# Optimization experiments

Hardware: AMD Instinct MI355X
Metric: run time of the kernel (lower is better)

Reference implementation:

```python
import jax, jax.numpy as jnp
import numpy as np

WS = 7           # window size
NH = 12          # num heads
EPS_ADA = 1e-6   # AdaLayerNorm eps
EPS_LN = 1e-5    # torch nn.LayerNorm default eps


def _rel_pos_index(ws):
    coords = np.stack(np.meshgrid(np.arange(ws), np.arange(ws), indexing='ij'))  # (2,ws,ws)
    flat = coords.reshape(2, -1)                      # (2, N)
    rel = flat[:, :, None] - flat[:, None, :]         # (2, N, N)
    rel = rel.transpose(1, 2, 0).astype(np.int64)     # (N, N, 2)
    rel[:, :, 0] += ws - 1
    rel[:, :, 1] += ws - 1
    rel[:, :, 0] *= 2 * ws - 1
    return jnp.asarray(rel.sum(-1))                   # (N, N) in [0, (2ws-1)^2)

REL_IDX = _rel_pos_index(WS)


def setup_inputs() -> dict:
    key = jax.random.key(0)
    ks = jax.random.split(key, 8)
    B, H, W, C, COND = 32, 56, 56, 384, 128
    L = H * W
    s = 0.02
    return {
        'x_tok': jax.random.normal(ks[0], (B, L, C), jnp.float32),
        'z_tok': jax.random.normal(ks[1], (B, L, C), jnp.float32),
        'cond': jax.random.normal(ks[2], (B, COND), jnp.float32),
        'gamma_x': jnp.ones((C,), jnp.float32),
        'beta_x': jnp.zeros((C,), jnp.float32),
        'mod_w': jax.random.normal(ks[3], (COND, 2 * C), jnp.float32) * s,
        'mod_b': jnp.zeros((2 * C,), jnp.float32),
        'gamma_z': jnp.ones((C,), jnp.float32),
        'beta_z': jnp.zeros((C,), jnp.float32),
        'rel_bias_table': jax.random.normal(ks[4], ((2 * WS - 1) ** 2, NH), jnp.float32) * s,
        'q_w': jax.random.normal(ks[5], (C, C), jnp.float32) * s,
        'q_b': jnp.zeros((C,), jnp.float32),
        'kv_w': jax.random.normal(ks[6], (C, 2 * C), jnp.float32) * s,
        'kv_b': jnp.zeros((2 * C,), jnp.float32),
        'proj_w': jax.random.normal(ks[7], (C, C), jnp.float32) * s,
        'proj_b': jnp.zeros((C,), jnp.float32),
        'H': H,
        'W': W,
    }


def reference(x_tok, z_tok, cond, gamma_x, beta_x, mod_w, mod_b,
              gamma_z, beta_z, rel_bias_table, q_w, q_b, kv_w, kv_b,
              proj_w, proj_b, H, W):
    B, L, C = x_tok.shape
    hd = C // NH
    N = WS * WS

    # AdaLayerNorm-Zero on x
    mu = x_tok.mean(-1, keepdims=True)
    var = ((x_tok - mu) ** 2).mean(-1, keepdims=True)
    x_hat = (x_tok - mu) * jax.lax.rsqrt(var + EPS_ADA)
    mod = (cond @ mod_w + mod_b).reshape(B, 2, C)
    d_gamma, d_beta = mod[:, 0], mod[:, 1]
    x = (gamma_x * (1.0 + d_gamma))[:, None, :] * x_hat + (beta_x + d_beta)[:, None, :]

    # LayerNorm on z
    mz = z_tok.mean(-1, keepdims=True)
    vz = ((z_tok - mz) ** 2).mean(-1, keepdims=True)
    z = (z_tok - mz) * jax.lax.rsqrt(vz + EPS_LN) * gamma_z + beta_z

    # window partition: (B,H,W,C) -> (B*nW, N, C)
    def part(t):
        t = t.reshape(B, H // WS, WS, W // WS, WS, C)
        return t.transpose(0, 1, 3, 2, 4, 5).reshape(-1, N, C)

    x_win = part(x.reshape(B, H, W, C))
    z_win = part(z.reshape(B, H, W, C))

    # cross window attention
    q = (x_win @ q_w + q_b).reshape(-1, N, NH, hd).transpose(0, 2, 1, 3)  # (Bw,H,N,d)
    kv = (z_win @ kv_w + kv_b).reshape(-1, N, 2, NH, hd)
    k = kv[:, :, 0].transpose(0, 2, 1, 3)
    v = kv[:, :, 1].transpose(0, 2, 1, 3)
    scale = hd ** -0.5
    attn = jnp.einsum('bhnd,bhmd->bhnm', q * scale, k)                    # (Bw,H,N,N)
    bias = rel_bias_table[REL_IDX.reshape(-1)].reshape(N, N, NH).transpose(2, 0, 1)
    attn = jax.nn.softmax(attn + bias[None], axis=-1)
    out = jnp.einsum('bhnm,bhmd->bhnd', attn, v).transpose(0, 2, 1, 3).reshape(-1, N, C)
    out = out @ proj_w + proj_b

    # window reverse: (B*nW, N, C) -> (B, L, C)
    fused = out.reshape(B, H // WS, W // WS, WS, WS, C)
    fused = fused.transpose(0, 1, 3, 2, 4, 5).reshape(B, L, C)

    return x_tok + fused
```

## Files before the change

### kernel.cpp

```cpp
#include <hip/hip_runtime.h>
#include <hip/hip_bf16.h>

typedef float f32x4 __attribute__((ext_vector_type(4)));
typedef short short8 __attribute__((ext_vector_type(8)));
typedef __hip_bfloat16 bf16;

constexpr int CDIM  = 384;
constexpr int LTOK  = 3136;
constexpr int NWIN  = 2048;
constexpr int MROWS = 100352;
constexpr int MPAD  = MROWS + 64;

__device__ __forceinline__ void gload_lds16(const void* g, void* l) {
  __builtin_amdgcn_global_load_lds(
      (const __attribute__((address_space(1))) void*)g,
      (__attribute__((address_space(3))) void*)l, 16, 0, 0);
}

__device__ __forceinline__ void row_to_bl(int r, int& b, int& l) {
  int w = r / 49, n = r % 49;
  b = w >> 6;
  int wrem = w & 63;
  int wy = wrem >> 3, wx = wrem & 7;
  int ny = n / 7, nx = n % 7;
  l = (wy * 7 + ny) * 56 + wx * 7 + nx;
}


__global__ __launch_bounds__(256) void mod_kernel(
    const float* __restrict__ cond, const float* __restrict__ mw,
    const float* __restrict__ mb, float* __restrict__ mod) {
  int idx = blockIdx.x * 256 + threadIdx.x;
  int b = idx / 768, j = idx % 768;
  float s = mb[j];
  const float* cr = cond + b * 128;
  #pragma unroll 4
  for (int k = 0; k < 128; k++) s += cr[k] * mw[(size_t)k * 768 + j];
  mod[idx] = s;
}

__global__ __launch_bounds__(256) void prep_wt(
    const float* __restrict__ qw, const float* __restrict__ kvw,
    const float* __restrict__ pw,
    bf16* __restrict__ wtq, bf16* __restrict__ wtkv, bf16* __restrict__ wtp) {
  int idx = blockIdx.x * 256 + threadIdx.x;
  const float* src; bf16* dst; int i, Wn;
  if (idx < 147456)      { i = idx;          src = qw;  dst = wtq;  Wn = 384; }
  else if (idx < 442368) { i = idx - 147456; src = kvw; dst = wtkv; Wn = 768; }
  else                   { i = idx - 442368; src = pw;  dst = wtp;  Wn = 384; }
  int j = i & 7, n = (i >> 3) & 63, g = (i >> 9) & 3;
  int kt = (i >> 11) % 12, chunk = i / 24576;
  int k = kt * 32 + g * 8 + j, ng = chunk * 64 + n;
  dst[i] = __float2bfloat16(src[(size_t)k * Wn + ng]);
}

__global__ __launch_bounds__(256) void bias_kernel(
    const float* __restrict__ tab, float* __restrict__ bT) {
  int idx = blockIdx.x * 256 + threadIdx.x;
  int h = idx >> 12, rem = idx & 4095, m = rem >> 6, c = rem & 63;
  float v;
  if (c >= 49)      v = -1e30f;
  else if (m >= 49) v = 0.f;
  else {
    int yq = m / 7, xq = m % 7, yk = c / 7, xk = c % 7;
    v = tab[((yq - yk + 6) * 13 + (xq - xk + 6)) * 12 + h];
  }
  bT[idx] = v;
}


struct alignas(8) B4 { bf16 h[4]; };

__global__ __launch_bounds__(256) void ln_kernel(
    const float* __restrict__ src, const float* __restrict__ gamma,
    const float* __restrict__ beta, const float* __restrict__ mod,
    float eps, bf16* __restrict__ dst) {
  int wid = threadIdx.x >> 6, lane = threadIdx.x & 63;
  int r = blockIdx.x * 4 + wid;
  int bb, ll; row_to_bl(r, bb, ll);
  const f32x4* x4 = (const f32x4*)(src + ((size_t)bb * LTOK + ll) * 384);
  f32x4 a = x4[lane];
  f32x4 b = {0.f, 0.f, 0.f, 0.f};
  if (lane < 32) b = x4[64 + lane];
  float s  = a[0] + a[1] + a[2] + a[3] + b[0] + b[1] + b[2] + b[3];
  float s2 = a[0]*a[0] + a[1]*a[1] + a[2]*a[2] + a[3]*a[3]
           + b[0]*b[0] + b[1]*b[1] + b[2]*b[2] + b[3]*b[3];
  #pragma unroll
  for (int d = 1; d < 64; d <<= 1) { s += __shfl_xor(s, d); s2 += __shfl_xor(s2, d); }
  float mu = s * (1.f / 384.f);
  float var = s2 * (1.f / 384.f) - mu * mu;
  float rstd = rsqrtf(var + eps);
  bf16* o = dst + (size_t)r * 384;
  const f32x4* g4 = (const f32x4*)gamma;
  const f32x4* be4 = (const f32x4*)beta;
  if (mod != nullptr) {
    const f32x4* mg4 = (const f32x4*)(mod + bb * 768);
    const f32x4* mb4 = (const f32x4*)(mod + bb * 768 + 384);
    {
      f32x4 gg = g4[lane], bb2 = be4[lane], mg = mg4[lane], mb = mb4[lane];
      B4 p;
      #pragma unroll
      for (int i = 0; i < 4; i++)
        p.h[i] = __float2bfloat16((gg[i] * (1.f + mg[i])) * ((a[i] - mu) * rstd) + bb2[i] + mb[i]);
      *((B4*)o + lane) = p;
    }
    if (lane < 32) {
      f32x4 gg = g4[64 + lane], bb2 = be4[64 + lane], mg = mg4[64 + lane], mb = mb4[64 + lane];
      B4 p;
      #pragma unroll
      for (int i = 0; i < 4; i++)
        p.h[i] = __float2bfloat16((gg[i] * (1.f + mg[i])) * ((b[i] - mu) * rstd) + bb2[i] + mb[i]);
      *((B4*)o + 64 + lane) = p;
    }
  } else {
    {
      f32x4 gg = g4[lane], bb2 = be4[lane];
      B4 p;
      #pragma unroll
      for (int i = 0; i < 4; i++)
        p.h[i] = __float2bfloat16((a[i] - mu) * rstd * gg[i] + bb2[i]);
      *((B4*)o + lane) = p;
    }
    if (lane < 32) {
      f32x4 gg = g4[64 + lane], bb2 = be4[64 + lane];
      B4 p;
      #pragma unroll
      for (int i = 0; i < 4; i++)
        p.h[i] = __float2bfloat16((b[i] - mu) * rstd * gg[i] + bb2[i]);
      *((B4*)o + 64 + lane) = p;
    }
  }
}


template<int MODE>
__global__ __launch_bounds__(256, 3) void gemm2(
    const bf16* __restrict__ A, const bf16* __restrict__ WTt,
    const float* __restrict__ bias, void* __restrict__ outp,
    const float* __restrict__ resid, float scale, int N) {
  __shared__ __align__(16) char Bs[49152];
  const int t = threadIdx.x;
  const int wid = t >> 6, lane = t & 63;
  const int r16 = lane & 15, g = lane >> 4;
  const int wr0 = blockIdx.x * 128 + wid * 32;

  short8 aF[2][12];
  #pragma unroll
  for (int m = 0; m < 2; m++)
    #pragma unroll
    for (int kt = 0; kt < 12; kt++)
      aF[m][kt] = *(const short8*)(A + (size_t)(wr0 + m * 16 + r16) * 384 + kt * 32 + g * 8);

  const int NCH = N >> 6;
  auto stage = [&](int c) {
    const char* srcp = (const char*)WTt + (size_t)c * 49152;
    #pragma unroll
    for (int i = 0; i < 12; i++)
      gload_lds16(srcp + (i * 256 + t) * 16, Bs + (i * 256 + t) * 16);
  };
  stage(0);

  for (int c = 0; c < NCH; c++) {
    __syncthreads();
    f32x4 acc[2][4] = {};
    #pragma unroll
    for (int kt = 0; kt < 12; kt++) {
      #pragma unroll
      for (int ni = 0; ni < 4; ni++) {
        short8 bF = *(const short8*)(Bs + kt * 4096 + g * 1024 + (ni * 16 + r16) * 16);
        acc[0][ni] = __builtin_amdgcn_mfma_f32_16x16x32_bf16(aF[0][kt], bF, acc[0][ni], 0, 0, 0);
        acc[1][ni] = __builtin_amdgcn_mfma_f32_16x16x32_bf16(aF[1][kt], bF, acc[1][ni], 0, 0, 0);
      }
    }
    __syncthreads();
    if (c + 1 < NCH) stage(c + 1);

    if (MODE == 0) {
      bf16* O = (bf16*)outp;
      #pragma unroll
      for (int ni = 0; ni < 4; ni++) {
        int col = c * 64 + ni * 16 + r16;
        float bc = bias[col];
        #pragma unroll
        for (int m = 0; m < 2; m++) {
          int row0 = wr0 + m * 16 + g * 4;
          #pragma unroll
          for (int rr = 0; rr < 4; rr++)
            O[(size_t)(row0 + rr) * N + col] = __float2bfloat16((acc[m][ni][rr] + bc) * scale);
        }
      }
    } else {
      float* O = (float*)outp;
      #pragma unroll
      for (int m = 0; m < 2; m++) {
        #pragma unroll
        for (int rr = 0; rr < 4; rr++) {
          int row = wr0 + m * 16 + g * 4 + rr;
          int bb, ll; row_to_bl(row, bb, ll);
          size_t base = ((size_t)bb * LTOK + ll) * 384;
          #pragma unroll
          for (int ni = 0; ni < 4; ni++) {
            int col = c * 64 + ni * 16 + r16;
            O[base + col] = resid[base + col] + acc[m][ni][rr] + bias[col];
          }
        }
      }
    }
  }
}


__global__ __launch_bounds__(64) void attn_kernel(
    const bf16* __restrict__ q, const bf16* __restrict__ kv,
    const float* __restrict__ biasT, bf16* __restrict__ o) {
  __shared__ __align__(16) bf16 vt[32][72];
  __shared__ __align__(16) bf16 P[64][72];
  const int h = blockIdx.x, w = blockIdx.y;
  const int lane = threadIdx.x;
  const int r16 = lane & 15, g = lane >> 4;
  const size_t qbase = (size_t)w * 49 * 384 + h * 32;
  const size_t kvbase = (size_t)w * 49 * 768 + h * 32;

  for (int e = lane; e < 32 * 72; e += 64) ((bf16*)vt)[e] = __float2bfloat16(0.f);
  for (int e = lane; e < 49 * 32; e += 64) {
    int c = e >> 5, d = e & 31;
    vt[d][c] = kv[kvbase + (size_t)c * 768 + 384 + d];
  }

  short8 aq[4], bk[4];
  #pragma unroll
  for (int mi = 0; mi < 4; mi++)
    aq[mi] = *(const short8*)(q + qbase + (size_t)(mi * 16 + r16) * 384 + g * 8);
  #pragma unroll
  for (int ni = 0; ni < 4; ni++)
    bk[ni] = *(const short8*)(kv + kvbase + (size_t)(ni * 16 + r16) * 768 + g * 8);

  f32x4 zero = {0.f, 0.f, 0.f, 0.f};
  f32x4 S[4][4];
  #pragma unroll
  for (int mi = 0; mi < 4; mi++)
    #pragma unroll
    for (int ni = 0; ni < 4; ni++)
      S[mi][ni] = __builtin_amdgcn_mfma_f32_16x16x32_bf16(aq[mi], bk[ni], zero, 0, 0, 0);

  const float* bt = biasT + h * 4096;
  #pragma unroll
  for (int mi = 0; mi < 4; mi++) {
    #pragma unroll
    for (int r = 0; r < 4; r++) {
      int rowm = mi * 16 + g * 4 + r;
      float sv[4];
      #pragma unroll
      for (int ni = 0; ni < 4; ni++)
        sv[ni] = S[mi][ni][r] + bt[rowm * 64 + ni * 16 + r16];
      float mx = fmaxf(fmaxf(sv[0], sv[1]), fmaxf(sv[2], sv[3]));
      #pragma unroll
      for (int d = 1; d < 16; d <<= 1) mx = fmaxf(mx, __shfl_xor(mx, d));
      float sum = 0.f;
      #pragma unroll
      for (int ni = 0; ni < 4; ni++) { sv[ni] = __expf(sv[ni] - mx); sum += sv[ni]; }
      #pragma unroll
      for (int d = 1; d < 16; d <<= 1) sum += __shfl_xor(sum, d);
      float inv = __fdividef(1.f, sum);
      #pragma unroll
      for (int ni = 0; ni < 4; ni++)
        P[rowm][ni * 16 + r16] = __float2bfloat16(sv[ni] * inv);
    }
  }
  __syncthreads();

  f32x4 acc[4][2] = {};
  #pragma unroll
  for (int c0 = 0; c0 < 2; c0++) {
    short8 ap[4], bv[2];
    #pragma unroll
    for (int mi = 0; mi < 4; mi++)
      ap[mi] = *(const short8*)((const char*)&P[0][0] + (mi * 16 + r16) * 144 + c0 * 64 + g * 16);
    #pragma unroll
    for (int di = 0; di < 2; di++)
      bv[di] = *(const short8*)((const char*)&vt[0][0] + (di * 16 + r16) * 144 + c0 * 64 + g * 16);
    #pragma unroll
    for (int mi = 0; mi < 4; mi++)
      #pragma unroll
      for (int di = 0; di < 2; di++)
        acc[mi][di] = __builtin_amdgcn_mfma_f32_16x16x32_bf16(ap[mi], bv[di], acc[mi][di], 0, 0, 0);
  }

  #pragma unroll
  for (int mi = 0; mi < 4; mi++) {
    #pragma unroll
    for (int r = 0; r < 4; r++) {
      int m = mi * 16 + g * 4 + r;
      if (m < 49) {
        #pragma unroll
        for (int di = 0; di < 2; di++)
          o[(size_t)(w * 49 + m) * 384 + h * 32 + di * 16 + r16] =
              __float2bfloat16(acc[mi][di][r]);
      }
    }
  }
}


extern "C" void kernel_launch(void* const* d_in, const int* in_sizes, int n_in,
                              void* d_out, int out_size, void* d_ws, size_t ws_size,
                              hipStream_t stream) {
  (void)in_sizes; (void)n_in; (void)out_size; (void)ws_size;
  const float* x_tok   = (const float*)d_in[0];
  const float* z_tok   = (const float*)d_in[1];
  const float* cond    = (const float*)d_in[2];
  const float* gamma_x = (const float*)d_in[3];
  const float* beta_x  = (const float*)d_in[4];
  const float* mod_w   = (const float*)d_in[5];
  const float* mod_b   = (const float*)d_in[6];
  const float* gamma_z = (const float*)d_in[7];
  const float* beta_z  = (const float*)d_in[8];
  const float* rel_tab = (const float*)d_in[9];
  const float* q_w     = (const float*)d_in[10];
  const float* q_b     = (const float*)d_in[11];
  const float* kv_w    = (const float*)d_in[12];
  const float* kv_b    = (const float*)d_in[13];
  const float* proj_w  = (const float*)d_in[14];
  const float* proj_b  = (const float*)d_in[15];

  char* ws = (char*)d_ws;
  float* modbuf = (float*)(ws + 0);
  bf16*  wtq    = (bf16*)(ws + 98304);
  bf16*  wtkv   = (bf16*)(ws + 98304 + 294912);
  bf16*  wtp    = (bf16*)(ws + 98304 + 294912 + 589824);
  float* biasT  = (float*)(ws + 98304 + 294912 + 589824 + 294912);
  char*  R1     = ws + 1474560;
  char*  R2     = R1 + (size_t)MPAD * 384 * 2;
  char*  R3     = R2 + (size_t)MPAD * 384 * 2;

  hipMemsetAsync(R2 + (size_t)MROWS * 384 * 2, 0, 64 * 384 * 2, stream);
  hipMemsetAsync(R3 + (size_t)MROWS * 768 * 2, 0, 64 * 768 * 2, stream);

  mod_kernel <<<96,   256, 0, stream>>>(cond, mod_w, mod_b, modbuf);
  prep_wt    <<<2304, 256, 0, stream>>>(q_w, kv_w, proj_w, wtq, wtkv, wtp);
  bias_kernel<<<192,  256, 0, stream>>>(rel_tab, biasT);

  ln_kernel<<<25088, 256, 0, stream>>>(x_tok, gamma_x, beta_x, modbuf, 1e-6f, (bf16*)R1);
  gemm2<0><<<784, 256, 0, stream>>>(
      (const bf16*)R1, wtq, q_b, R2, nullptr, 0.17677669529663687f, 384);
  ln_kernel<<<25088, 256, 0, stream>>>(z_tok, gamma_z, beta_z, nullptr, 1e-5f, (bf16*)R1);
  gemm2<0><<<784, 256, 0, stream>>>(
      (const bf16*)R1, wtkv, kv_b, R3, nullptr, 1.0f, 768);
  attn_kernel<<<dim3(12, NWIN), 64, 0, stream>>>(
      (const bf16*)R2, (const bf16*)R3, biasT, (bf16*)R1);
  gemm2<1><<<784, 256, 0, stream>>>(
      (const bf16*)R1, wtp, proj_b, d_out, x_tok, 1.0f, 384);
}
```

Baseline: 656.0 us.

## Double-buffer weight chunks in GEMM with 32-column tiles and LDS bias

The GEMM kernel now streams 32-column weight chunks into two alternating LDS buffers, prefetching the next chunk before computing the current one. Manual vmcnt waits and raw barriers replace the syncthreads pair, so the weight loads can overlap the MFMA work and the epilogue stores. The bias is also cached in LDS, and the weight-prep layout is changed to match the new chunking. The cost is more loop iterations with fewer MFMAs each, and vmcnt counts that must exactly match the number of outstanding epilogue stores.

```diff
diff --git a/kernel.cpp b/kernel.cpp
--- a/kernel.cpp
+++ b/kernel.cpp
@@ -48,10 +48,11 @@
   if (idx < 147456)      { i = idx;          src = qw;  dst = wtq;  Wn = 384; }
   else if (idx < 442368) { i = idx - 147456; src = kvw; dst = wtkv; Wn = 768; }
   else                   { i = idx - 442368; src = pw;  dst = wtp;  Wn = 384; }
-  int j = i & 7, n = (i >> 3) & 63, g = (i >> 9) & 3;
-  int kt = (i >> 11) % 12, chunk = i / 24576;
-  int k = kt * 32 + g * 8 + j, ng = chunk * 64 + n;
-  dst[i] = __float2bfloat16(src[(size_t)k * Wn + ng]);
+  int chunk = i / 12288, rem = i % 12288;
+  int kt = rem >> 10, rem2 = rem & 1023;
+  int ni = (rem2 >> 9) & 1, g = (rem2 >> 7) & 3, r16 = (rem2 >> 3) & 15, j = rem2 & 7;
+  int k = kt * 32 + g * 8 + j, n = chunk * 32 + ni * 16 + r16;
+  dst[i] = __float2bfloat16(src[(size_t)k * Wn + n]);
 }
 
 __global__ __launch_bounds__(256) void bias_kernel(
@@ -134,11 +135,12 @@
 
 
 template<int MODE>
-__global__ __launch_bounds__(256, 3) void gemm2(
+__global__ __launch_bounds__(256, 3) void gemm3(
     const bf16* __restrict__ A, const bf16* __restrict__ WTt,
     const float* __restrict__ bias, void* __restrict__ outp,
     const float* __restrict__ resid, float scale, int N) {
-  __shared__ __align__(16) char Bs[49152];
+  __shared__ __align__(16) char Bs[2][24576];
+  __shared__ float biasS[768];
   const int t = threadIdx.x;
   const int wid = t >> 6, lane = t & 63;
   const int r16 = lane & 15, g = lane >> 4;
@@ -151,36 +153,54 @@
     for (int kt = 0; kt < 12; kt++)
       aF[m][kt] = *(const short8*)(A + (size_t)(wr0 + m * 16 + r16) * 384 + kt * 32 + g * 8);
 
-  const int NCH = N >> 6;
-  auto stage = [&](int c) {
-    const char* srcp = (const char*)WTt + (size_t)c * 49152;
-    #pragma unroll
-    for (int i = 0; i < 12; i++)
-      gload_lds16(srcp + (i * 256 + t) * 16, Bs + (i * 256 + t) * 16);
+  #pragma unroll
+  for (int i = 0; i < 3; i++) {
+    int idx = i * 256 + t;
+    if (idx < N) biasS[idx] = bias[idx];
+  }
+
+  const int NCH = N >> 5;
+  auto stage = [&](int c, int pb) {
+    const char* srcp = (const char*)WTt + (size_t)c * 24576;
+    #pragma unroll
+    for (int i = 0; i < 6; i++)
+      gload_lds16(srcp + i * 4096 + t * 16, Bs[pb] + i * 4096 + t * 16);
   };
-  stage(0);
-
-  for (int c = 0; c < NCH; c++) {
-    __syncthreads();
-    f32x4 acc[2][4] = {};
+  stage(0, 0);
+  __syncthreads();
+
+  constexpr int EPI = (MODE == 0) ? 16 : 32;
+
+  for (int c = 0; c < NCH; ++c) {
+    if (c + 1 < NCH) {
+      stage(c + 1, (c + 1) & 1);
+      asm volatile("s_waitcnt vmcnt(%0)" :: "i"(EPI + 6) : "memory");
+    } else {
+      asm volatile("s_waitcnt vmcnt(%0)" :: "i"(EPI) : "memory");
+    }
+    __builtin_amdgcn_s_barrier();
+    __builtin_amdgcn_sched_barrier(0);
+
+    const char* bufp = Bs[c & 1];
+    f32x4 acc[2][2] = {};
     #pragma unroll
     for (int kt = 0; kt < 12; kt++) {
-      #pragma unroll
-      for (int ni = 0; ni < 4; ni++) {
-        short8 bF = *(const short8*)(Bs + kt * 4096 + g * 1024 + (ni * 16 + r16) * 16);
-        acc[0][ni] = __builtin_amdgcn_mfma_f32_16x16x32_bf16(aF[0][kt], bF, acc[0][ni], 0, 0, 0);
-        acc[1][ni] = __builtin_amdgcn_mfma_f32_16x16x32_bf16(aF[1][kt], bF, acc[1][ni], 0, 0, 0);
-      }
-    }
-    __syncthreads();
-    if (c + 1 < NCH) stage(c + 1);
+      short8 b0 = *(const short8*)(bufp + kt * 2048 + g * 256 + r16 * 16);
+      short8 b1 = *(const short8*)(bufp + kt * 2048 + 1024 + g * 256 + r16 * 16);
+      acc[0][0] = __builtin_amdgcn_mfma_f32_16x16x32_bf16(aF[0][kt], b0, acc[0][0], 0, 0, 0);
+      acc[1][0] = __builtin_amdgcn_mfma_f32_16x16x32_bf16(aF[1][kt], b0, acc[1][0], 0, 0, 0);
+      acc[0][1] = __builtin_amdgcn_mfma_f32_16x16x32_bf16(aF[0][kt], b1, acc[0][1], 0, 0, 0);
+      acc[1][1] = __builtin_amdgcn_mfma_f32_16x16x32_bf16(aF[1][kt], b1, acc[1][1], 0, 0, 0);
+    }
+    __builtin_amdgcn_sched_barrier(0);
+    __builtin_amdgcn_s_barrier();
 
     if (MODE == 0) {
       bf16* O = (bf16*)outp;
       #pragma unroll
-      for (int ni = 0; ni < 4; ni++) {
-        int col = c * 64 + ni * 16 + r16;
-        float bc = bias[col];
+      for (int ni = 0; ni < 2; ni++) {
+        int col = c * 32 + ni * 16 + r16;
+        float bc = biasS[col];
         #pragma unroll
         for (int m = 0; m < 2; m++) {
           int row0 = wr0 + m * 16 + g * 4;
@@ -199,9 +219,9 @@
           int bb, ll; row_to_bl(row, bb, ll);
           size_t base = ((size_t)bb * LTOK + ll) * 384;
           #pragma unroll
-          for (int ni = 0; ni < 4; ni++) {
-            int col = c * 64 + ni * 16 + r16;
-            O[base + col] = resid[base + col] + acc[m][ni][rr] + bias[col];
+          for (int ni = 0; ni < 2; ni++) {
+            int col = c * 32 + ni * 16 + r16;
+            O[base + col] = resid[base + col] + acc[m][ni][rr] + biasS[col];
           }
         }
       }
@@ -341,13 +361,13 @@
   bias_kernel<<<192,  256, 0, stream>>>(rel_tab, biasT);
 
   ln_kernel<<<25088, 256, 0, stream>>>(x_tok, gamma_x, beta_x, modbuf, 1e-6f, (bf16*)R1);
-  gemm2<0><<<784, 256, 0, stream>>>(
+  gemm3<0><<<784, 256, 0, stream>>>(
       (const bf16*)R1, wtq, q_b, R2, nullptr, 0.17677669529663687f, 384);
   ln_kernel<<<25088, 256, 0, stream>>>(z_tok, gamma_z, beta_z, nullptr, 1e-5f, (bf16*)R1);
-  gemm2<0><<<784, 256, 0, stream>>>(
+  gemm3<0><<<784, 256, 0, stream>>>(
       (const bf16*)R1, wtkv, kv_b, R3, nullptr, 1.0f, 768);
   attn_kernel<<<dim3(12, NWIN), 64, 0, stream>>>(
       (const bf16*)R2, (const bf16*)R3, biasT, (bf16*)R1);
-  gemm2<1><<<784, 256, 0, stream>>>(
+  gemm3<1><<<784, 256, 0, stream>>>(
       (const bf16*)R1, wtp, proj_b, d_out, x_tok, 1.0f, 384);
 }
```

Measured after the change: 614.4 us. 1.07x faster.

## Make GEMM blocks weight-stationary and merge prep and layernorm launches

Applied to the files above, without the earlier changes.

The GEMM is restructured so each block loads one 64-column weight slice into LDS once. It then loops persistently over 64-row panels of A, reading A fragments from global memory each iteration, instead of holding 128 rows of A in registers and streaming every weight chunk through LDS with barriers. The three prep kernels are merged into one launch, and the two layernorms into one launch writing separate buffers, which cuts launch count and lets the x and z normalizations run concurrently. The trade-off is that A is re-read from global memory once per column slice (6 or 12 times) instead of once, relying on L2 to absorb it, while occupancy rises to 4 blocks per CU.

```diff
diff --git a/kernel.cpp b/kernel.cpp
--- a/kernel.cpp
+++ b/kernel.cpp
@@ -10,6 +10,7 @@
 constexpr int NWIN  = 2048;
 constexpr int MROWS = 100352;
 constexpr int MPAD  = MROWS + 64;
+constexpr int NP64  = 1568;
 
 __device__ __forceinline__ void gload_lds16(const void* g, void* l) {
   __builtin_amdgcn_global_load_lds(
@@ -27,56 +28,67 @@
 }
 
 
-__global__ __launch_bounds__(256) void mod_kernel(
+__global__ __launch_bounds__(256) void prep_all(
     const float* __restrict__ cond, const float* __restrict__ mw,
-    const float* __restrict__ mb, float* __restrict__ mod) {
-  int idx = blockIdx.x * 256 + threadIdx.x;
-  int b = idx / 768, j = idx % 768;
-  float s = mb[j];
-  const float* cr = cond + b * 128;
-  #pragma unroll 4
-  for (int k = 0; k < 128; k++) s += cr[k] * mw[(size_t)k * 768 + j];
-  mod[idx] = s;
-}
-
-__global__ __launch_bounds__(256) void prep_wt(
+    const float* __restrict__ mb, float* __restrict__ mod,
     const float* __restrict__ qw, const float* __restrict__ kvw,
     const float* __restrict__ pw,
-    bf16* __restrict__ wtq, bf16* __restrict__ wtkv, bf16* __restrict__ wtp) {
-  int idx = blockIdx.x * 256 + threadIdx.x;
-  const float* src; bf16* dst; int i, Wn;
-  if (idx < 147456)      { i = idx;          src = qw;  dst = wtq;  Wn = 384; }
-  else if (idx < 442368) { i = idx - 147456; src = kvw; dst = wtkv; Wn = 768; }
-  else                   { i = idx - 442368; src = pw;  dst = wtp;  Wn = 384; }
-  int j = i & 7, n = (i >> 3) & 63, g = (i >> 9) & 3;
-  int kt = (i >> 11) % 12, chunk = i / 24576;
-  int k = kt * 32 + g * 8 + j, ng = chunk * 64 + n;
-  dst[i] = __float2bfloat16(src[(size_t)k * Wn + ng]);
-}
-
-__global__ __launch_bounds__(256) void bias_kernel(
+    bf16* __restrict__ wtq, bf16* __restrict__ wtkv, bf16* __restrict__ wtp,
     const float* __restrict__ tab, float* __restrict__ bT) {
-  int idx = blockIdx.x * 256 + threadIdx.x;
-  int h = idx >> 12, rem = idx & 4095, m = rem >> 6, c = rem & 63;
-  float v;
-  if (c >= 49)      v = -1e30f;
-  else if (m >= 49) v = 0.f;
-  else {
-    int yq = m / 7, xq = m % 7, yk = c / 7, xk = c % 7;
-    v = tab[((yq - yk + 6) * 13 + (xq - xk + 6)) * 12 + h];
-  }
-  bT[idx] = v;
+  int bid = blockIdx.x, t = threadIdx.x;
+  if (bid < 96) {
+    int idx = bid * 256 + t;
+    int b = idx / 768, j = idx % 768;
+    float s = mb[j];
+    const float* cr = cond + b * 128;
+    #pragma unroll 4
+    for (int k = 0; k < 128; k++) s += cr[k] * mw[(size_t)k * 768 + j];
+    mod[idx] = s;
+  } else if (bid < 2400) {
+    int idx = (bid - 96) * 256 + t;
+    const float* src; bf16* dst; int i, Wn;
+    if (idx < 147456)      { i = idx;          src = qw;  dst = wtq;  Wn = 384; }
+    else if (idx < 442368) { i = idx - 147456; src = kvw; dst = wtkv; Wn = 768; }
+    else                   { i = idx - 442368; src = pw;  dst = wtp;  Wn = 384; }
+    int j = i & 7, nc = (i >> 3) & 63, g = (i >> 9) & 3;
+    int kt = (i >> 11) % 12, s = i / 24576;
+    int k = kt * 32 + g * 8 + j, n = s * 64 + nc;
+    dst[i] = __float2bfloat16(src[(size_t)k * Wn + n]);
+  } else {
+    int idx = (bid - 2400) * 256 + t;
+    int h = idx >> 12, rem = idx & 4095, m = rem >> 6, c = rem & 63;
+    float v;
+    if (c >= 49)      v = -1e30f;
+    else if (m >= 49) v = 0.f;
+    else {
+      int yq = m / 7, xq = m % 7, yk = c / 7, xk = c % 7;
+      v = tab[((yq - yk + 6) * 13 + (xq - xk + 6)) * 12 + h];
+    }
+    bT[idx] = v;
+  }
 }
 
 
 struct alignas(8) B4 { bf16 h[4]; };
 
-__global__ __launch_bounds__(256) void ln_kernel(
-    const float* __restrict__ src, const float* __restrict__ gamma,
-    const float* __restrict__ beta, const float* __restrict__ mod,
-    float eps, bf16* __restrict__ dst) {
+__global__ __launch_bounds__(256) void ln_both(
+    const float* __restrict__ x_tok, const float* __restrict__ gx,
+    const float* __restrict__ bx, const float* __restrict__ modbuf,
+    const float* __restrict__ z_tok, const float* __restrict__ gz,
+    const float* __restrict__ bz,
+    bf16* __restrict__ xO, bf16* __restrict__ zO) {
+  int bid = blockIdx.x;
+  bool isX = bid < 25088;
+  const float* src   = isX ? x_tok : z_tok;
+  const float* gamma = isX ? gx : gz;
+  const float* beta  = isX ? bx : bz;
+  const float* mod   = isX ? modbuf : nullptr;
+  bf16* dst          = isX ? xO : zO;
+  float eps          = isX ? 1e-6f : 1e-5f;
+  int rb = (isX ? bid : bid - 25088) * 4;
+
   int wid = threadIdx.x >> 6, lane = threadIdx.x & 63;
-  int r = blockIdx.x * 4 + wid;
+  int r = rb + wid;
   int bb, ll; row_to_bl(r, bb, ll);
   const f32x4* x4 = (const f32x4*)(src + ((size_t)bb * LTOK + ll) * 384);
   f32x4 a = x4[lane];
@@ -134,76 +146,64 @@
 
 
 template<int MODE>
-__global__ __launch_bounds__(256, 3) void gemm2(
+__global__ __launch_bounds__(256, 4) void gemm6(
     const bf16* __restrict__ A, const bf16* __restrict__ WTt,
     const float* __restrict__ bias, void* __restrict__ outp,
-    const float* __restrict__ resid, float scale, int N) {
-  __shared__ __align__(16) char Bs[49152];
+    const float* __restrict__ resid, float scale, int N, int NS, int BPS) {
+  __shared__ __align__(16) bf16 wS[24576];
   const int t = threadIdx.x;
   const int wid = t >> 6, lane = t & 63;
   const int r16 = lane & 15, g = lane >> 4;
-  const int wr0 = blockIdx.x * 128 + wid * 32;
-
-  short8 aF[2][12];
-  #pragma unroll
-  for (int m = 0; m < 2; m++)
+  const int s = blockIdx.x % NS, bi = blockIdx.x / NS;
+
+  {
+    const char* src = (const char*)WTt + (size_t)s * 49152;
+    #pragma unroll
+    for (int i = 0; i < 12; i++)
+      gload_lds16(src + (i * 256 + t) * 16, (char*)wS + (i * 256 + t) * 16);
+  }
+  float bc[4];
+  #pragma unroll
+  for (int ni = 0; ni < 4; ni++) bc[ni] = bias[s * 64 + ni * 16 + r16];
+  __syncthreads();
+
+  for (int p = bi; p < NP64; p += BPS) {
+    const int prow = p * 64 + wid * 16;
+
+    short8 aF[12];
     #pragma unroll
     for (int kt = 0; kt < 12; kt++)
-      aF[m][kt] = *(const short8*)(A + (size_t)(wr0 + m * 16 + r16) * 384 + kt * 32 + g * 8);
-
-  const int NCH = N >> 6;
-  auto stage = [&](int c) {
-    const char* srcp = (const char*)WTt + (size_t)c * 49152;
-    #pragma unroll
-    for (int i = 0; i < 12; i++)
-      gload_lds16(srcp + (i * 256 + t) * 16, Bs + (i * 256 + t) * 16);
-  };
-  stage(0);
-
-  for (int c = 0; c < NCH; c++) {
-    __syncthreads();
-    f32x4 acc[2][4] = {};
+      aF[kt] = *(const short8*)(A + (size_t)(prow + r16) * 384 + kt * 32 + g * 8);
+
+    f32x4 acc[4] = {};
     #pragma unroll
     for (int kt = 0; kt < 12; kt++) {
       #pragma unroll
       for (int ni = 0; ni < 4; ni++) {
-        short8 bF = *(const short8*)(Bs + kt * 4096 + g * 1024 + (ni * 16 + r16) * 16);
-        acc[0][ni] = __builtin_amdgcn_mfma_f32_16x16x32_bf16(aF[0][kt], bF, acc[0][ni], 0, 0, 0);
-        acc[1][ni] = __builtin_amdgcn_mfma_f32_16x16x32_bf16(aF[1][kt], bF, acc[1][ni], 0, 0, 0);
+        short8 wF = *(const short8*)((const char*)wS + (kt * 4 + g) * 1024 + (ni * 16 + r16) * 16);
+        acc[ni] = __builtin_amdgcn_mfma_f32_16x16x32_bf16(aF[kt], wF, acc[ni], 0, 0, 0);
       }
     }
-    __syncthreads();
-    if (c + 1 < NCH) stage(c + 1);
 
     if (MODE == 0) {
       bf16* O = (bf16*)outp;
       #pragma unroll
-      for (int ni = 0; ni < 4; ni++) {
-        int col = c * 64 + ni * 16 + r16;
-        float bc = bias[col];
+      for (int rr = 0; rr < 4; rr++) {
+        size_t rbase = (size_t)(prow + g * 4 + rr) * N + s * 64;
         #pragma unroll
-        for (int m = 0; m < 2; m++) {
-          int row0 = wr0 + m * 16 + g * 4;
-          #pragma unroll
-          for (int rr = 0; rr < 4; rr++)
-            O[(size_t)(row0 + rr) * N + col] = __float2bfloat16((acc[m][ni][rr] + bc) * scale);
-        }
+        for (int ni = 0; ni < 4; ni++)
+          O[rbase + ni * 16 + r16] = __float2bfloat16((acc[ni][rr] + bc[ni]) * scale);
       }
     } else {
       float* O = (float*)outp;
       #pragma unroll
-      for (int m = 0; m < 2; m++) {
+      for (int rr = 0; rr < 4; rr++) {
+        int row = prow + g * 4 + rr;
+        int bb, ll; row_to_bl(row, bb, ll);
+        size_t base = ((size_t)bb * LTOK + ll) * 384 + s * 64;
         #pragma unroll
-        for (int rr = 0; rr < 4; rr++) {
-          int row = wr0 + m * 16 + g * 4 + rr;
-          int bb, ll; row_to_bl(row, bb, ll);
-          size_t base = ((size_t)bb * LTOK + ll) * 384;
-          #pragma unroll
-          for (int ni = 0; ni < 4; ni++) {
-            int col = c * 64 + ni * 16 + r16;
-            O[base + col] = resid[base + col] + acc[m][ni][rr] + bias[col];
-          }
-        }
+        for (int ni = 0; ni < 4; ni++)
+          O[base + ni * 16 + r16] = resid[base + ni * 16 + r16] + acc[ni][rr] + bc[ni];
       }
     }
   }
@@ -332,22 +332,23 @@
   char*  R1     = ws + 1474560;
   char*  R2     = R1 + (size_t)MPAD * 384 * 2;
   char*  R3     = R2 + (size_t)MPAD * 384 * 2;
+  char*  R4     = R3 + (size_t)MPAD * 768 * 2;
 
   hipMemsetAsync(R2 + (size_t)MROWS * 384 * 2, 0, 64 * 384 * 2, stream);
   hipMemsetAsync(R3 + (size_t)MROWS * 768 * 2, 0, 64 * 768 * 2, stream);
 
-  mod_kernel <<<96,   256, 0, stream>>>(cond, mod_w, mod_b, modbuf);
-  prep_wt    <<<2304, 256, 0, stream>>>(q_w, kv_w, proj_w, wtq, wtkv, wtp);
-  bias_kernel<<<192,  256, 0, stream>>>(rel_tab, biasT);
-
-  ln_kernel<<<25088, 256, 0, stream>>>(x_tok, gamma_x, beta_x, modbuf, 1e-6f, (bf16*)R1);
-  gemm2<0><<<784, 256, 0, stream>>>(
-      (const bf16*)R1, wtq, q_b, R2, nullptr, 0.17677669529663687f, 384);
-  ln_kernel<<<25088, 256, 0, stream>>>(z_tok, gamma_z, beta_z, nullptr, 1e-5f, (bf16*)R1);
-  gemm2<0><<<784, 256, 0, stream>>>(
-      (const bf16*)R1, wtkv, kv_b, R3, nullptr, 1.0f, 768);
+  prep_all<<<2592, 256, 0, stream>>>(cond, mod_w, mod_b, modbuf,
+                                     q_w, kv_w, proj_w, wtq, wtkv, wtp,
+                                     rel_tab, biasT);
+  ln_both<<<50176, 256, 0, stream>>>(x_tok, gamma_x, beta_x, modbuf,
+                                     z_tok, gamma_z, beta_z,
+                                     (bf16*)R1, (bf16*)R4);
+  gemm6<0><<<768, 256, 0, stream>>>(
+      (const bf16*)R1, wtq, q_b, R2, nullptr, 0.17677669529663687f, 384, 6, 128);
+  gemm6<0><<<768, 256, 0, stream>>>(
+      (const bf16*)R4, wtkv, kv_b, R3, nullptr, 1.0f, 768, 12, 64);
   attn_kernel<<<dim3(12, NWIN), 64, 0, stream>>>(
       (const bf16*)R2, (const bf16*)R3, biasT, (bf16*)R1);
-  gemm2<1><<<784, 256, 0, stream>>>(
-      (const bf16*)R1, wtp, proj_b, d_out, x_tok, 1.0f, 384);
-}
+  gemm6<1><<<768, 256, 0, stream>>>(
+      (const bf16*)R1, wtp, proj_b, d_out, x_tok, 1.0f, 384, 6, 128);
+}
```

Result: slower. 704.6 us (+7.4%).
